# Performance work log

Hardware: AMD Instinct MI355X
Metric: run time of the kernel (lower is better)

Reference implementation:

```python
import jax, jax.numpy as jnp
import numpy as np

B, T, D, H, L, OUT, FC = 256, 512, 64, 256, 2, 1, 128


def setup_inputs() -> dict:
    key = jax.random.key(0)
    ks = jax.random.split(key, 16)
    s = 1.0 / np.sqrt(H)
    u = lambda k, shape: jax.random.uniform(k, shape, jnp.float32, -s, s)
    return {
        "x": jax.random.normal(ks[0], (B, T, D), jnp.float32),
        # layer 0 LSTM params (PyTorch gate order: i, f, g, o)
        "W_ih0": u(ks[1], (4 * H, D)),
        "W_hh0": u(ks[2], (4 * H, H)),
        "b_ih0": u(ks[3], (4 * H,)),
        "b_hh0": u(ks[4], (4 * H,)),
        # layer 1 LSTM params
        "W_ih1": u(ks[5], (4 * H, H)),
        "W_hh1": u(ks[6], (4 * H, H)),
        "b_ih1": u(ks[7], (4 * H,)),
        "b_hh1": u(ks[8], (4 * H,)),
        # MLP head
        "fc1_w": u(ks[9], (FC, H)),
        "fc1_b": u(ks[10], (FC,)),
        "fc2_w": u(ks[11], (OUT, FC)),
        "fc2_b": u(ks[12], (OUT,)),
    }


def _lstm_layer(x, W_ih, W_hh, b_ih, b_hh):
    # x: [B, T, Din] -> (outputs [B, T, H], final hidden [B, H])
    Bsz = x.shape[0]
    Hh = W_hh.shape[1]
    # precompute input contribution to all gates: [B, T, 4H]
    xg = jnp.einsum("btd,gd->btg", x, W_ih) + b_ih + b_hh

    def step(carry, xt):
        h, c = carry
        g = xt + h @ W_hh.T  # [B, 4H]
        i, f, gg, o = jnp.split(g, 4, axis=-1)
        i = jax.nn.sigmoid(i)
        f = jax.nn.sigmoid(f)
        gg = jnp.tanh(gg)
        o = jax.nn.sigmoid(o)
        c = f * c + i * gg
        h = o * jnp.tanh(c)
        return (h, c), h

    h0 = jnp.zeros((Bsz, Hh), x.dtype)
    (hT, _cT), hs = jax.lax.scan(step, (h0, h0), jnp.swapaxes(xg, 0, 1))
    return jnp.swapaxes(hs, 0, 1), hT


def reference(x, W_ih0, W_hh0, b_ih0, b_hh0, W_ih1, W_hh1, b_ih1, b_hh1,
              fc1_w, fc1_b, fc2_w, fc2_b):
    # eval-mode forward: inter-layer dropout (p=0.2) is a no-op
    y0, h0f = _lstm_layer(x, W_ih0, W_hh0, b_ih0, b_hh0)
    _y1, h1f = _lstm_layer(y0, W_ih1, W_hh1, b_ih1, b_hh1)
    # h_n.view(-1, H): stack per-layer final hidden states -> [L*B, H]
    h_n = jnp.concatenate([h0f, h1f], axis=0)
    out = jax.nn.relu(h_n)
    out = jax.nn.relu(out @ fc1_w.T + fc1_b)
    return out @ fc2_w.T + fc2_b  # [L*B, OUT]
```

## Files before the change

### kernel.cpp

```cpp
#include <hip/hip_runtime.h>

#define Bb 256
#define Tt 512
#define Dd 64
#define Hh 256
#define NP 16
#define HB2 (256 * 256)
#define FSTRIDE 16

typedef unsigned short u16;
typedef _Float16 f16;
typedef __attribute__((ext_vector_type(8))) _Float16 f16x8;
typedef __attribute__((ext_vector_type(4))) _Float16 f16x4;
typedef __attribute__((ext_vector_type(4))) float f32x4;
typedef __attribute__((ext_vector_type(4))) unsigned int u32x4;

__device__ __forceinline__ f16x8 bc8h(u32x4 v) { return __builtin_bit_cast(f16x8, v); }

__device__ __forceinline__ float fsig(float x) {
  x = fminf(fmaxf(x, -30.f), 30.f);
  return 1.f / (1.f + __expf(-x));
}
__device__ __forceinline__ float ftanh(float x) {
  x = fminf(fmaxf(x, -15.f), 15.f);
  float t = __expf(2.f * x);
  return (t - 1.f) / (t + 1.f);
}

__device__ __forceinline__ f16x8 ld16_sc1(const f16* p) {
  f16x8 r;
  asm volatile("global_load_dwordx4 %0, %1, off sc1" : "=v"(r) : "v"(p) : "memory");
  return r;
}
__device__ __forceinline__ f16x8 ld16_sc0(const f16* p) {
  f16x8 r;
  asm volatile("global_load_dwordx4 %0, %1, off sc0" : "=v"(r) : "v"(p) : "memory");
  return r;
}
__device__ __forceinline__ void st2_sc1(f16* p, unsigned v) {
  asm volatile("global_store_short %0, %1, off sc1" : : "v"(p), "v"(v) : "memory");
}
__device__ __forceinline__ void st2_plain(f16* p, unsigned v) {
  asm volatile("global_store_short %0, %1, off" : : "v"(p), "v"(v) : "memory");
}
__device__ __forceinline__ void st4u_plain(unsigned* p, unsigned v) {
  asm volatile("global_store_dword %0, %1, off" : : "v"(p), "v"(v) : "memory");
}
__device__ __forceinline__ void st4u_sc1(unsigned* p, unsigned v) {
  asm volatile("global_store_dword %0, %1, off sc1" : : "v"(p), "v"(v) : "memory");
}
__device__ __forceinline__ unsigned ld4_sc0(const unsigned* p) {
  unsigned r;
  asm volatile("global_load_dword %0, %1, off sc0\n\ts_waitcnt vmcnt(0)"
               : "=v"(r) : "v"(p) : "memory");
  return r;
}

__global__ __launch_bounds__(256) void prep_x(const float* __restrict__ x,
                                              f16* __restrict__ xh) {
  int i = blockIdx.x * blockDim.x + threadIdx.x;
  const int n4 = Bb * Tt * Dd / 4;
  if (i >= n4) return;
  f32x4 v = ((const f32x4*)x)[i];
  f16x4 o;
#pragma unroll
  for (int j = 0; j < 4; ++j) o[j] = (f16)v[j];
  ((f16x4*)xh)[i] = o;
}

__global__ __launch_bounds__(256) void prep_w(
    const float* __restrict__ wih0, const float* __restrict__ whh0,
    const float* __restrict__ bih0, const float* __restrict__ bhh0,
    const float* __restrict__ wih1, const float* __restrict__ whh1,
    const float* __restrict__ bih1, const float* __restrict__ bhh1,
    f16* __restrict__ wfrag, float* __restrict__ bias0s, float* __restrict__ bias1s) {
  int tid = blockIdx.x * blockDim.x + threadIdx.x;
  int np = gridDim.x * blockDim.x;
  const int tot = 16 * 8 * 32 * 512;
  for (int u = tid; u < tot; u += np) {
    int e = u & 7, l = (u >> 3) & 63;
    int f = (u >> 9) & 31;
    int wv = (u >> 14) & 7;
    int p = u >> 17;
    int g = wv & 3;
    int grow = g * 256 + p * 16 + (l & 15);
    int klane = (l >> 4) * 8 + e;
    float w = 0.f;
    if (wv < 4) {
      if (f < 4)       w = wih0[grow * 64 + (f >> 1) * 32 + klane];
      else if (f < 20) w = whh0[grow * 256 + ((f - 4) >> 1) * 32 + klane];
    } else {
      if (f < 16)      w = wih1[grow * 256 + (f >> 1) * 32 + klane];
      else             w = whh1[grow * 256 + ((f - 16) >> 1) * 32 + klane];
    }
    f16 hi = (f16)w;
    wfrag[u] = (f & 1) ? (f16)((w - (float)hi) * 2048.0f) : hi;
  }
  for (int u = tid; u < 1024; u += np) {
    bias0s[u] = bih0[u] + bhh0[u];
    bias1s[u] = bih1[u] + bhh1[u];
  }
}

#define MF(A, B, C) __builtin_amdgcn_mfma_f32_16x16x32_f16(A, B, C, 0, 0, 0)

__global__ __launch_bounds__(512, 1) void lstm_persist(
    const f16* __restrict__ xh, const f16* __restrict__ wfrag,
    const float* __restrict__ bias0s, const float* __restrict__ bias1s,
    f16* h0, f16* h1, unsigned* flags, unsigned* probe, unsigned* verdict) {
  const int bid = blockIdx.x;
  const int p = (bid >> 3) & 15;
  const int grp = (bid & 7) * 2 + (bid >> 7);
  const int tid = threadIdx.x;
  const int wv = tid >> 6, lane = tid & 63;
  const int lr = lane & 15, lk = lane >> 4;
  const int g = wv & 3;
  const bool isL1 = wv >= 4;
  const float LOSCALE = 1.0f / 2048.0f;

  __shared__ float gbuf[2][4][16][16];
  __shared__ u32x4 hbuf[2][16][36];
  __shared__ unsigned s_fast;

  f16x8 wf[32];
  {
    const u32x4* wp = (const u32x4*)wfrag + ((size_t)(p * 8 + wv) * 32) * 64 + lane;
#pragma unroll
    for (int f = 0; f < 20; ++f) wf[f] = bc8h(wp[(size_t)f * 64]);
    if (isL1) {
#pragma unroll
      for (int f = 20; f < 32; ++f) wf[f] = bc8h(wp[(size_t)f * 64]);
    }
  }
  const float bias = (isL1 ? bias1s : bias0s)[g * 256 + p * 16 + lr];

  if (tid < 256) {
    int lsel = tid >> 7;
    int d = tid & 127;
    int row = d >> 3, cp = d & 7;
    f16* base = lsel ? h1 : (h0 + (size_t)3 * HB2);
    unsigned* w = (unsigned*)(base + (size_t)(grp * 16 + row) * 256 + p * 16) + cp;
    st4u_plain(w, 0u);
    st4u_sc1(w, 0u);
  }
  asm volatile("s_waitcnt vmcnt(0)" ::: "memory");
  __syncthreads();

  if (wv == 0) {
    if (lane == 0) {
      st4u_plain(&probe[grp * NP + p], (unsigned)(p + 1));
      asm volatile("s_waitcnt vmcnt(0)" ::: "memory");
    }
    bool seen = (lane >= NP);
    bool ok;
    int it = 0;
    while (true) {
      if (!seen) {
        unsigned got = ld4_sc0(&probe[grp * NP + lane]);
        if (got == (unsigned)(lane + 1)) seen = true;
      }
      if (__all(seen)) { ok = true; break; }
      if (++it > 768) { ok = false; break; }
      __builtin_amdgcn_s_sleep(2);
    }
    if (lane == 0)
      __hip_atomic_store(&verdict[grp * NP + p], ok ? 1u : 2u, __ATOMIC_RELAXED,
                         __HIP_MEMORY_SCOPE_AGENT);
    unsigned v;
    while (true) {
      v = 1u;
      if (lane < NP)
        v = __hip_atomic_load(&verdict[grp * NP + lane], __ATOMIC_RELAXED,
                              __HIP_MEMORY_SCOPE_AGENT);
      if (!__any(v == 0u)) break;
      __builtin_amdgcn_s_sleep(2);
    }
    if (lane == 0) s_fast = __any(v != 1u) ? 0u : 1u;
  }
  __syncthreads();
  const bool fast = (s_fast != 0u);

  const int eL = tid >> 8;
  const int erow = (tid >> 4) & 15, ecol = tid & 15;
  float c = 0.f;
  f16* const hout = ((eL ? h1 : h0) + (size_t)(grp * 16 + erow) * 256 + p * 16 + ecol);

  const int hrow = grp * 16 + lr;
  const f16* xbase = xh + (size_t)hrow * Tt * Dd + lk * 8;
  const f16* hsrcbase = ((wv < 4) ? h0 : h1) + (size_t)grp * 4096;
  const int hlsel = wv >> 2;

  for (int k = 0; k <= Tt; ++k) {
    f32x4 a = (f32x4){bias, bias, bias, bias};
    f32x4 b = (f32x4){0.f, 0.f, 0.f, 0.f};
    if (!isL1 && k < Tt) {
      const u32x4* xp = (const u32x4*)(xbase + (size_t)k * Dd);
      f16x8 xf0 = bc8h(xp[0]);
      f16x8 xf1 = bc8h(xp[4]);
      a = MF(xf0, wf[0], a);
      b = MF(xf0, wf[1], b);
      a = MF(xf1, wf[2], a);
      b = MF(xf1, wf[3], b);
    }

    if (wv == 0) {
      bool ready = false;
      while (!ready) {
        unsigned v = 0xFFFFFFFFu;
        if (lane < NP)
          v = __hip_atomic_load(&flags[(grp * NP + lane) * FSTRIDE],
                                __ATOMIC_RELAXED, __HIP_MEMORY_SCOPE_AGENT);
        ready = !__any(v < (unsigned)k);
        if (!ready) __builtin_amdgcn_s_sleep(1);
      }
    }
    asm volatile("" ::: "memory");
    __syncthreads();

    const int par = (k - 1) & 3;

    {
      const f16* src = hsrcbase + (size_t)par * HB2;
      const int j0 = (wv & 3) * 2;
      const f16* p0 = src + j0 * 512 + lane * 8;
      f16x8 s0, s1;
      if (fast) {
        s0 = ld16_sc0(p0);
        s1 = ld16_sc0(p0 + 512);
      } else {
        s0 = ld16_sc1(p0);
        s1 = ld16_sc1(p0 + 512);
      }
      asm volatile("s_waitcnt vmcnt(0)" ::: "memory");
      const int r0 = j0 * 2 + (lane >> 5);
      const int c2 = lane & 31;
      hbuf[hlsel][r0][c2 ^ (r0 & 7)] = __builtin_bit_cast(u32x4, s0);
      hbuf[hlsel][r0 + 2][c2 ^ ((r0 + 2) & 7)] = __builtin_bit_cast(u32x4, s1);
    }
    __syncthreads();

    f16x8 A0[8], A1[8];
#pragma unroll
    for (int kt = 0; kt < 8; ++kt)
      A0[kt] = __builtin_bit_cast(f16x8, hbuf[0][lr][(kt * 4 + lk) ^ (lr & 7)]);
    if (isL1) {
#pragma unroll
      for (int kt = 0; kt < 8; ++kt)
        A1[kt] = __builtin_bit_cast(f16x8, hbuf[1][lr][(kt * 4 + lk) ^ (lr & 7)]);
    }

    if (!isL1) {
      if (k < Tt) {
#pragma unroll
        for (int kt = 0; kt < 8; ++kt) {
          a = MF(A0[kt], wf[4 + 2 * kt], a);
          b = MF(A0[kt], wf[5 + 2 * kt], b);
        }
        a += b * LOSCALE;
#pragma unroll
        for (int r = 0; r < 4; ++r) gbuf[0][g][lk * 4 + r][lr] = a[r];
      }
    } else if (k >= 1) {
#pragma unroll
      for (int kt = 0; kt < 8; ++kt) {
        a = MF(A0[kt], wf[2 * kt], a);
        b = MF(A0[kt], wf[2 * kt + 1], b);
      }
#pragma unroll
      for (int kt = 0; kt < 8; ++kt) {
        a = MF(A1[kt], wf[16 + 2 * kt], a);
        b = MF(A1[kt], wf[17 + 2 * kt], b);
      }
      a += b * LOSCALE;
#pragma unroll
      for (int r = 0; r < 4; ++r) gbuf[1][g][lk * 4 + r][lr] = a[r];
    }
    __syncthreads();

    {
      const bool upd = eL ? (k >= 1) : (k < Tt);
      if (upd) {
        float iv = fsig(gbuf[eL][0][erow][ecol]);
        float fv = fsig(gbuf[eL][1][erow][ecol]);
        float gv = ftanh(gbuf[eL][2][erow][ecol]);
        float ov = fsig(gbuf[eL][3][erow][ecol]);
        c = fv * c + iv * gv;
        float hval = ov * ftanh(c);
        f16 fh = (f16)hval;
        unsigned bits = (unsigned)__builtin_bit_cast(u16, fh);
        f16* Ho = hout + (size_t)(k & 3) * HB2;
        if (fast) st2_plain(Ho, bits);
        else      st2_sc1(Ho, bits);
      }
    }
    asm volatile("s_waitcnt vmcnt(0)" ::: "memory");
    __syncthreads();
    if (tid == 0)
      __hip_atomic_store(&flags[(grp * NP + p) * FSTRIDE], (unsigned)(k + 1),
                         __ATOMIC_RELAXED, __HIP_MEMORY_SCOPE_AGENT);
  }
}

__global__ __launch_bounds__(128) void head_kernel(
    const f16* __restrict__ h0f, const f16* __restrict__ h1f,
    const float* __restrict__ fc1w, const float* __restrict__ fc1b,
    const float* __restrict__ fc2w, const float* __restrict__ fc2b,
    float* __restrict__ out) {
  int r = blockIdx.x;
  const f16* hh = (r < 256) ? (h0f + r * Hh) : (h1f + (r - 256) * Hh);
  __shared__ float v[Hh];
  int tid = threadIdx.x;
  for (int i = tid; i < Hh; i += 128)
    v[i] = fmaxf((float)hh[i], 0.f);
  __syncthreads();
  float s = fc1b[tid];
#pragma unroll 8
  for (int i = 0; i < Hh; ++i) s += fc1w[tid * Hh + i] * v[i];
  s = fmaxf(s, 0.f) * fc2w[tid];
#pragma unroll
  for (int off = 32; off; off >>= 1) s += __shfl_down(s, off);
  __shared__ float red[2];
  if ((tid & 63) == 0) red[tid >> 6] = s;
  __syncthreads();
  if (tid == 0) out[r] = red[0] + red[1] + fc2b[0];
}

extern "C" void kernel_launch(void* const* d_in, const int* in_sizes, int n_in,
                              void* d_out, int out_size, void* d_ws, size_t ws_size,
                              hipStream_t stream) {
  (void)in_sizes; (void)n_in; (void)out_size; (void)ws_size;
  const float* x    = (const float*)d_in[0];
  const float* wih0 = (const float*)d_in[1];
  const float* whh0 = (const float*)d_in[2];
  const float* bih0 = (const float*)d_in[3];
  const float* bhh0 = (const float*)d_in[4];
  const float* wih1 = (const float*)d_in[5];
  const float* whh1 = (const float*)d_in[6];
  const float* bih1 = (const float*)d_in[7];
  const float* bhh1 = (const float*)d_in[8];
  const float* fc1w = (const float*)d_in[9];
  const float* fc1b = (const float*)d_in[10];
  const float* fc2w = (const float*)d_in[11];
  const float* fc2b = (const float*)d_in[12];

  char* ws = (char*)d_ws;
  size_t off = 0;
  f16* xh = (f16*)(ws + off); off += (size_t)Bb * Tt * Dd * 2;
  f16* wfrag = (f16*)(ws + off); off += (size_t)16 * 8 * 32 * 512 * 2;
  float* bias0s = (float*)(ws + off); off += 4096;
  float* bias1s = (float*)(ws + off); off += 4096;
  char* zbase = ws + off;
  f16* h0 = (f16*)(ws + off); off += (size_t)4 * HB2 * 2;
  f16* h1 = (f16*)(ws + off); off += (size_t)4 * HB2 * 2;
  unsigned* flags = (unsigned*)(ws + off); off += 256 * FSTRIDE * 4;
  unsigned* probe = (unsigned*)(ws + off); off += 1024;
  unsigned* verdict = (unsigned*)(ws + off); off += 1024;
  size_t zbytes = (size_t)((ws + off) - zbase);

  hipMemsetAsync(zbase, 0, zbytes, stream);
  prep_x<<<Bb * Tt * Dd / 4 / 256, 256, 0, stream>>>(x, xh);
  prep_w<<<512, 256, 0, stream>>>(wih0, whh0, bih0, bhh0, wih1, whh1, bih1, bhh1,
                                  wfrag, bias0s, bias1s);
  lstm_persist<<<256, 512, 0, stream>>>(xh, wfrag, bias0s, bias1s, h0, h1, flags,
                                        probe, verdict);
  head_kernel<<<512, 128, 0, stream>>>(h0 + (size_t)3 * HB2, h1, fc1w, fc1b,
                                       fc2w, fc2b, (float*)d_out);
}
```

Before: 1.521 ms.

## Split layer-0 and layer-1 LSTM work into separate persistent blocks

Launches 512 blocks of 256 threads instead of 256 blocks of 512, giving layer 0 and layer 1 their own blocks with separate progress flags. Layer-0 blocks may run up to three steps ahead of layer 1 (bounded by the 4-slot h ring), so the two layers pipeline instead of sharing one barrier per step. MFMA chains are also split into two independent accumulators to shorten dependency chains. The cost is more blocks that must be co-resident for the spin-wait scheme, more flag polling traffic, and a bounded-spin escape that could break correctness if the timeout is ever hit.

```diff
diff --git a/kernel.cpp b/kernel.cpp
--- a/kernel.cpp
+++ b/kernel.cpp
@@ -104,41 +104,43 @@
 
 #define MF(A, B, C) __builtin_amdgcn_mfma_f32_16x16x32_f16(A, B, C, 0, 0, 0)
 
-__global__ __launch_bounds__(512, 1) void lstm_persist(
+__global__ __launch_bounds__(256, 2) void lstm_persist(
     const f16* __restrict__ xh, const f16* __restrict__ wfrag,
     const float* __restrict__ bias0s, const float* __restrict__ bias1s,
-    f16* h0, f16* h1, unsigned* flags, unsigned* probe, unsigned* verdict) {
+    f16* h0, f16* h1, unsigned* h0flags, unsigned* l1flags, unsigned* probe,
+    unsigned* verdict) {
   const int bid = blockIdx.x;
-  const int p = (bid >> 3) & 15;
-  const int grp = (bid & 7) * 2 + (bid >> 7);
+  const bool L1blk = bid >= 256;
+  const int b = bid & 255;
+  const int p = (b >> 3) & 15;
+  const int grp = (b & 7) * 2 + (b >> 7);
   const int tid = threadIdx.x;
   const int wv = tid >> 6, lane = tid & 63;
   const int lr = lane & 15, lk = lane >> 4;
-  const int g = wv & 3;
-  const bool isL1 = wv >= 4;
+  const int g = wv;
   const float LOSCALE = 1.0f / 2048.0f;
-
-  __shared__ float gbuf[2][4][16][16];
+  const int NPP = 32;
+
+  __shared__ float gbuf[4][16][16];
   __shared__ u32x4 hbuf[2][16][36];
   __shared__ unsigned s_fast;
 
   f16x8 wf[32];
   {
-    const u32x4* wp = (const u32x4*)wfrag + ((size_t)(p * 8 + wv) * 32) * 64 + lane;
+    const u32x4* wp =
+        (const u32x4*)wfrag + ((size_t)(p * 8 + (L1blk ? 4 + g : g)) * 32) * 64 + lane;
 #pragma unroll
     for (int f = 0; f < 20; ++f) wf[f] = bc8h(wp[(size_t)f * 64]);
-    if (isL1) {
+    if (L1blk) {
 #pragma unroll
       for (int f = 20; f < 32; ++f) wf[f] = bc8h(wp[(size_t)f * 64]);
     }
   }
-  const float bias = (isL1 ? bias1s : bias0s)[g * 256 + p * 16 + lr];
-
-  if (tid < 256) {
-    int lsel = tid >> 7;
-    int d = tid & 127;
-    int row = d >> 3, cp = d & 7;
-    f16* base = lsel ? h1 : (h0 + (size_t)3 * HB2);
+  const float bias = (L1blk ? bias1s : bias0s)[g * 256 + p * 16 + lr];
+
+  if (tid < 128) {
+    int row = tid >> 3, cp = tid & 7;
+    f16* base = L1blk ? h1 : (h0 + (size_t)3 * HB2);
     unsigned* w = (unsigned*)(base + (size_t)(grp * 16 + row) * 256 + p * 16) + cp;
     st4u_plain(w, 0u);
     st4u_sc1(w, 0u);
@@ -147,30 +149,32 @@
   __syncthreads();
 
   if (wv == 0) {
+    const int myslot = grp * NPP + (L1blk ? 16 : 0) + p;
+    const unsigned mytok = (unsigned)((L1blk ? 16 : 0) + p + 1);
     if (lane == 0) {
-      st4u_plain(&probe[grp * NP + p], (unsigned)(p + 1));
+      st4u_plain(&probe[myslot], mytok);
       asm volatile("s_waitcnt vmcnt(0)" ::: "memory");
     }
-    bool seen = (lane >= NP);
+    bool seen = (lane >= NPP);
     bool ok;
     int it = 0;
     while (true) {
       if (!seen) {
-        unsigned got = ld4_sc0(&probe[grp * NP + lane]);
+        unsigned got = ld4_sc0(&probe[grp * NPP + lane]);
         if (got == (unsigned)(lane + 1)) seen = true;
       }
       if (__all(seen)) { ok = true; break; }
-      if (++it > 768) { ok = false; break; }
+      if (++it > 1536) { ok = false; break; }
       __builtin_amdgcn_s_sleep(2);
     }
     if (lane == 0)
-      __hip_atomic_store(&verdict[grp * NP + p], ok ? 1u : 2u, __ATOMIC_RELAXED,
+      __hip_atomic_store(&verdict[myslot], ok ? 1u : 2u, __ATOMIC_RELAXED,
                          __HIP_MEMORY_SCOPE_AGENT);
     unsigned v;
     while (true) {
       v = 1u;
-      if (lane < NP)
-        v = __hip_atomic_load(&verdict[grp * NP + lane], __ATOMIC_RELAXED,
+      if (lane < NPP)
+        v = __hip_atomic_load(&verdict[grp * NPP + lane], __ATOMIC_RELAXED,
                               __HIP_MEMORY_SCOPE_AGENT);
       if (!__any(v == 0u)) break;
       __builtin_amdgcn_s_sleep(2);
@@ -180,38 +184,53 @@
   __syncthreads();
   const bool fast = (s_fast != 0u);
 
-  const int eL = tid >> 8;
-  const int erow = (tid >> 4) & 15, ecol = tid & 15;
+  const int erow = tid >> 4, ecol = tid & 15;
   float c = 0.f;
-  f16* const hout = ((eL ? h1 : h0) + (size_t)(grp * 16 + erow) * 256 + p * 16 + ecol);
+  f16* const hout =
+      (L1blk ? h1 : h0) + (size_t)(grp * 16 + erow) * 256 + p * 16 + ecol;
 
   const int hrow = grp * 16 + lr;
   const f16* xbase = xh + (size_t)hrow * Tt * Dd + lk * 8;
-  const f16* hsrcbase = ((wv < 4) ? h0 : h1) + (size_t)grp * 4096;
-  const int hlsel = wv >> 2;
-
-  for (int k = 0; k <= Tt; ++k) {
-    f32x4 a = (f32x4){bias, bias, bias, bias};
-    f32x4 b = (f32x4){0.f, 0.f, 0.f, 0.f};
-    if (!isL1 && k < Tt) {
+  const f16* h0src = h0 + (size_t)grp * 4096;
+  const f16* h1src = h1 + (size_t)grp * 4096;
+
+  for (int s = 0; s < Tt; ++s) {
+    const int k = s + (L1blk ? 1 : 0);
+
+    f32x4 a0 = (f32x4){bias, bias, bias, bias};
+    f32x4 b0 = (f32x4){0.f, 0.f, 0.f, 0.f};
+    f32x4 a1 = (f32x4){0.f, 0.f, 0.f, 0.f};
+    f32x4 b1 = (f32x4){0.f, 0.f, 0.f, 0.f};
+    if (!L1blk) {
       const u32x4* xp = (const u32x4*)(xbase + (size_t)k * Dd);
       f16x8 xf0 = bc8h(xp[0]);
       f16x8 xf1 = bc8h(xp[4]);
-      a = MF(xf0, wf[0], a);
-      b = MF(xf0, wf[1], b);
-      a = MF(xf1, wf[2], a);
-      b = MF(xf1, wf[3], b);
+      a0 = MF(xf0, wf[0], a0);
+      b0 = MF(xf0, wf[1], b0);
+      a1 = MF(xf1, wf[2], a1);
+      b1 = MF(xf1, wf[3], b1);
     }
 
     if (wv == 0) {
+      const unsigned thrA = (unsigned)k;
+      const unsigned thrB =
+          L1blk ? (unsigned)(k - 1) : (unsigned)(k >= 3 ? k - 3 : 0);
+      int it = 0;
       bool ready = false;
       while (!ready) {
         unsigned v = 0xFFFFFFFFu;
         if (lane < NP)
-          v = __hip_atomic_load(&flags[(grp * NP + lane) * FSTRIDE],
+          v = __hip_atomic_load(&h0flags[(grp * NP + lane) * FSTRIDE],
                                 __ATOMIC_RELAXED, __HIP_MEMORY_SCOPE_AGENT);
-        ready = !__any(v < (unsigned)k);
-        if (!ready) __builtin_amdgcn_s_sleep(1);
+        else if (lane < 2 * NP)
+          v = __hip_atomic_load(&l1flags[(grp * NP + lane - NP) * FSTRIDE],
+                                __ATOMIC_RELAXED, __HIP_MEMORY_SCOPE_AGENT);
+        const unsigned thr = (lane < NP) ? thrA : thrB;
+        ready = !__any(v < thr);
+        if (!ready) {
+          if (++it > 65536) break;
+          __builtin_amdgcn_s_sleep(1);
+        }
       }
     }
     asm volatile("" ::: "memory");
@@ -220,84 +239,97 @@
     const int par = (k - 1) & 3;
 
     {
-      const f16* src = hsrcbase + (size_t)par * HB2;
-      const int j0 = (wv & 3) * 2;
-      const f16* p0 = src + j0 * 512 + lane * 8;
-      f16x8 s0, s1;
+      const int j0 = wv * 2;
+      const f16* p00 = h0src + (size_t)par * HB2 + j0 * 512 + lane * 8;
+      f16x8 s0, s1, t0, t1;
       if (fast) {
-        s0 = ld16_sc0(p0);
-        s1 = ld16_sc0(p0 + 512);
+        s0 = ld16_sc0(p00);
+        s1 = ld16_sc0(p00 + 512);
       } else {
-        s0 = ld16_sc1(p0);
-        s1 = ld16_sc1(p0 + 512);
+        s0 = ld16_sc1(p00);
+        s1 = ld16_sc1(p00 + 512);
+      }
+      if (L1blk) {
+        const f16* p10 = h1src + (size_t)par * HB2 + j0 * 512 + lane * 8;
+        if (fast) {
+          t0 = ld16_sc0(p10);
+          t1 = ld16_sc0(p10 + 512);
+        } else {
+          t0 = ld16_sc1(p10);
+          t1 = ld16_sc1(p10 + 512);
+        }
       }
       asm volatile("s_waitcnt vmcnt(0)" ::: "memory");
       const int r0 = j0 * 2 + (lane >> 5);
       const int c2 = lane & 31;
-      hbuf[hlsel][r0][c2 ^ (r0 & 7)] = __builtin_bit_cast(u32x4, s0);
-      hbuf[hlsel][r0 + 2][c2 ^ ((r0 + 2) & 7)] = __builtin_bit_cast(u32x4, s1);
+      hbuf[0][r0][c2 ^ (r0 & 7)] = __builtin_bit_cast(u32x4, s0);
+      hbuf[0][r0 + 2][c2 ^ ((r0 + 2) & 7)] = __builtin_bit_cast(u32x4, s1);
+      if (L1blk) {
+        hbuf[1][r0][c2 ^ (r0 & 7)] = __builtin_bit_cast(u32x4, t0);
+        hbuf[1][r0 + 2][c2 ^ ((r0 + 2) & 7)] = __builtin_bit_cast(u32x4, t1);
+      }
     }
     __syncthreads();
 
-    f16x8 A0[8], A1[8];
+    f16x8 A0[8];
 #pragma unroll
     for (int kt = 0; kt < 8; ++kt)
       A0[kt] = __builtin_bit_cast(f16x8, hbuf[0][lr][(kt * 4 + lk) ^ (lr & 7)]);
-    if (isL1) {
+    if (!L1blk) {
+#pragma unroll
+      for (int kt = 0; kt < 8; kt += 2) {
+        a0 = MF(A0[kt], wf[4 + 2 * kt], a0);
+        b0 = MF(A0[kt], wf[5 + 2 * kt], b0);
+        a1 = MF(A0[kt + 1], wf[6 + 2 * kt], a1);
+        b1 = MF(A0[kt + 1], wf[7 + 2 * kt], b1);
+      }
+    } else {
+      f16x8 A1[8];
 #pragma unroll
       for (int kt = 0; kt < 8; ++kt)
         A1[kt] = __builtin_bit_cast(f16x8, hbuf[1][lr][(kt * 4 + lk) ^ (lr & 7)]);
-    }
-
-    if (!isL1) {
-      if (k < Tt) {
-#pragma unroll
-        for (int kt = 0; kt < 8; ++kt) {
-          a = MF(A0[kt], wf[4 + 2 * kt], a);
-          b = MF(A0[kt], wf[5 + 2 * kt], b);
-        }
-        a += b * LOSCALE;
-#pragma unroll
-        for (int r = 0; r < 4; ++r) gbuf[0][g][lk * 4 + r][lr] = a[r];
-      }
-    } else if (k >= 1) {
-#pragma unroll
-      for (int kt = 0; kt < 8; ++kt) {
-        a = MF(A0[kt], wf[2 * kt], a);
-        b = MF(A0[kt], wf[2 * kt + 1], b);
-      }
-#pragma unroll
-      for (int kt = 0; kt < 8; ++kt) {
-        a = MF(A1[kt], wf[16 + 2 * kt], a);
-        b = MF(A1[kt], wf[17 + 2 * kt], b);
-      }
-      a += b * LOSCALE;
-#pragma unroll
-      for (int r = 0; r < 4; ++r) gbuf[1][g][lk * 4 + r][lr] = a[r];
+#pragma unroll
+      for (int kt = 0; kt < 8; kt += 2) {
+        a0 = MF(A0[kt], wf[2 * kt], a0);
+        b0 = MF(A0[kt], wf[2 * kt + 1], b0);
+        a1 = MF(A0[kt + 1], wf[2 * kt + 2], a1);
+        b1 = MF(A0[kt + 1], wf[2 * kt + 3], b1);
+      }
+#pragma unroll
+      for (int kt = 0; kt < 8; kt += 2) {
+        a0 = MF(A1[kt], wf[16 + 2 * kt], a0);
+        b0 = MF(A1[kt], wf[17 + 2 * kt], b0);
+        a1 = MF(A1[kt + 1], wf[18 + 2 * kt], a1);
+        b1 = MF(A1[kt + 1], wf[19 + 2 * kt], b1);
+      }
+    }
+    {
+      f32x4 acc = (a0 + a1) + (b0 + b1) * LOSCALE;
+#pragma unroll
+      for (int r = 0; r < 4; ++r) gbuf[g][lk * 4 + r][lr] = acc[r];
     }
     __syncthreads();
 
     {
-      const bool upd = eL ? (k >= 1) : (k < Tt);
-      if (upd) {
-        float iv = fsig(gbuf[eL][0][erow][ecol]);
-        float fv = fsig(gbuf[eL][1][erow][ecol]);
-        float gv = ftanh(gbuf[eL][2][erow][ecol]);
-        float ov = fsig(gbuf[eL][3][erow][ecol]);
-        c = fv * c + iv * gv;
-        float hval = ov * ftanh(c);
-        f16 fh = (f16)hval;
-        unsigned bits = (unsigned)__builtin_bit_cast(u16, fh);
-        f16* Ho = hout + (size_t)(k & 3) * HB2;
-        if (fast) st2_plain(Ho, bits);
-        else      st2_sc1(Ho, bits);
-      }
+      float iv = fsig(gbuf[0][erow][ecol]);
+      float fv = fsig(gbuf[1][erow][ecol]);
+      float gv = ftanh(gbuf[2][erow][ecol]);
+      float ov = fsig(gbuf[3][erow][ecol]);
+      c = fv * c + iv * gv;
+      float hval = ov * ftanh(c);
+      f16 fh = (f16)hval;
+      unsigned bits = (unsigned)__builtin_bit_cast(u16, fh);
+      f16* Ho = hout + (size_t)(k & 3) * HB2;
+      if (fast) st2_plain(Ho, bits);
+      else      st2_sc1(Ho, bits);
     }
     asm volatile("s_waitcnt vmcnt(0)" ::: "memory");
     __syncthreads();
-    if (tid == 0)
-      __hip_atomic_store(&flags[(grp * NP + p) * FSTRIDE], (unsigned)(k + 1),
-                         __ATOMIC_RELAXED, __HIP_MEMORY_SCOPE_AGENT);
+    if (tid == 0) {
+      unsigned* fp = (L1blk ? l1flags : h0flags) + (grp * NP + p) * FSTRIDE;
+      unsigned nv = (unsigned)(L1blk ? k : k + 1);
+      __hip_atomic_store(fp, nv, __ATOMIC_RELAXED, __HIP_MEMORY_SCOPE_AGENT);
+    }
   }
 }
 
@@ -352,17 +384,18 @@
   char* zbase = ws + off;
   f16* h0 = (f16*)(ws + off); off += (size_t)4 * HB2 * 2;
   f16* h1 = (f16*)(ws + off); off += (size_t)4 * HB2 * 2;
-  unsigned* flags = (unsigned*)(ws + off); off += 256 * FSTRIDE * 4;
-  unsigned* probe = (unsigned*)(ws + off); off += 1024;
-  unsigned* verdict = (unsigned*)(ws + off); off += 1024;
+  unsigned* h0flags = (unsigned*)(ws + off); off += 256 * FSTRIDE * 4;
+  unsigned* l1flags = (unsigned*)(ws + off); off += 256 * FSTRIDE * 4;
+  unsigned* probe = (unsigned*)(ws + off); off += 2048;
+  unsigned* verdict = (unsigned*)(ws + off); off += 2048;
   size_t zbytes = (size_t)((ws + off) - zbase);
 
   hipMemsetAsync(zbase, 0, zbytes, stream);
   prep_x<<<Bb * Tt * Dd / 4 / 256, 256, 0, stream>>>(x, xh);
   prep_w<<<512, 256, 0, stream>>>(wih0, whh0, bih0, bhh0, wih1, whh1, bih1, bhh1,
                                   wfrag, bias0s, bias1s);
-  lstm_persist<<<256, 512, 0, stream>>>(xh, wfrag, bias0s, bias1s, h0, h1, flags,
-                                        probe, verdict);
+  lstm_persist<<<512, 256, 0, stream>>>(xh, wfrag, bias0s, bias1s, h0, h1,
+                                        h0flags, l1flags, probe, verdict);
   head_kernel<<<512, 128, 0, stream>>>(h0 + (size_t)3 * HB2, h1, fc1w, fc1b,
                                        fc2w, fc2b, (float*)d_out);
 }
```

New measurement: 1.606 ms. 5.6% more time.
